# Performance work log

Hardware: AMD Instinct MI355X
Metric: run time of the kernel (lower is better)

Reference implementation:

```python
import jax, jax.numpy as jnp
import numpy as np


def _lstm_layer(x, w_ih, w_hh, b):
    """Single LSTM layer, PyTorch gate order (i, f, g, o).
    x: [B, T, Din]; w_ih: [4H, Din]; w_hh: [4H, H]; b: [4H] (= b_ih + b_hh).
    Returns hidden states [B, T, H]."""
    H = w_hh.shape[1]
    # Precompute input contribution for all timesteps at once (big GEMM).
    gates_x = jnp.einsum('btd,gd->btg', x, w_ih) + b  # [B, T, 4H]
    gates_t = jnp.swapaxes(gates_x, 0, 1)             # [T, B, 4H]
    B = x.shape[0]
    h0 = jnp.zeros((B, H), x.dtype)
    c0 = jnp.zeros((B, H), x.dtype)

    def step(carry, gx):
        h, c = carry
        g = gx + h @ w_hh.T                           # [B, 4H]
        i, f, gg, o = jnp.split(g, 4, axis=-1)
        i = jax.nn.sigmoid(i)
        f = jax.nn.sigmoid(f)
        gg = jnp.tanh(gg)
        o = jax.nn.sigmoid(o)
        c = f * c + i * gg
        h = o * jnp.tanh(c)
        return (h, c), h

    _, hs = jax.lax.scan(step, (h0, c0), gates_t)     # hs: [T, B, H]
    return jnp.swapaxes(hs, 0, 1)                     # [B, T, H]


def setup_inputs() -> dict:
    key = jax.random.key(0)
    ks = jax.random.split(key, 10)
    B, T, Din = 256, 256, 128
    Hemb = 512   # hidden_size (embed output)
    H = 512      # lstm_hidden_size
    L = 3        # nlayers
    Dout = 1     # output_size

    def unif(k, shape, bound):
        return jax.random.uniform(k, shape, jnp.float32, -bound, bound)

    s_emb = 1.0 / np.sqrt(Din)
    s_lstm = 1.0 / np.sqrt(H)
    s_dec = 1.0 / np.sqrt(H)

    return {
        'x': jax.random.normal(ks[0], (B, T, Din), jnp.float32),
        'embed_W': unif(ks[1], (Hemb, Din), s_emb),
        'embed_b': unif(ks[2], (Hemb,), s_emb),
        # stacked per-layer LSTM weights (hidden_size == lstm_hidden_size)
        'w_ih': unif(ks[3], (L, 4 * H, Hemb), s_lstm),
        'w_hh': unif(ks[4], (L, 4 * H, H), s_lstm),
        'b_ih': unif(ks[5], (L, 4 * H), s_lstm),
        'b_hh': unif(ks[6], (L, 4 * H), s_lstm),
        'dec_W': unif(ks[7], (Dout, H), s_dec),
        'dec_b': unif(ks[8], (Dout,), s_dec),
    }


def reference(x, embed_W, embed_b, w_ih, w_hh, b_ih, b_hh, dec_W, dec_b):
    # embed: Linear(input_size -> hidden_size)
    h = x @ embed_W.T + embed_b                       # [B, T, Hemb]
    # multi-layer LSTM (batch_first), zero initial state
    L = w_ih.shape[0]
    for l in range(L):
        h = _lstm_layer(h, w_ih[l], w_hh[l], b_ih[l] + b_hh[l])
    # decoder on last timestep, then flatten
    out = h[:, -1] @ dec_W.T + dec_b                  # [B, Dout]
    return out.reshape(-1)
```

## Files before the change

kernel.cpp:

```cpp
#include <hip/hip_runtime.h>
#include <hip/hip_fp16.h>
#include <cstdint>


#define TT   256
#define NBAT 256
#define DIN  128
#define HID  512

typedef _Float16 half_t;
typedef __attribute__((ext_vector_type(8))) _Float16 half8;
typedef __attribute__((ext_vector_type(4))) _Float16 half4v;
typedef __attribute__((ext_vector_type(4))) float f32x4;

__device__ __forceinline__ float sigmoidf_(float x) {
    return 1.f / (1.f + __expf(-x));
}
__device__ __forceinline__ float tanhf_(float x) {
    float xc = fminf(fmaxf(x, -15.f), 15.f);
    float e = __expf(2.f * xc);
    return (e - 1.f) / (e + 1.f);
}

__device__ __forceinline__ half8 ld_cg16(const half_t* p) {
    union { unsigned long long u[2]; half8 v; } r;
    r.u[0] = __hip_atomic_load((const unsigned long long*)p,
                               __ATOMIC_RELAXED, __HIP_MEMORY_SCOPE_AGENT);
    r.u[1] = __hip_atomic_load((const unsigned long long*)p + 1,
                               __ATOMIC_RELAXED, __HIP_MEMORY_SCOPE_AGENT);
    return r.v;
}
__device__ __forceinline__ void st_cg2(half_t* p, float v) {
    half_t h = (half_t)v;
    unsigned short b = __builtin_bit_cast(unsigned short, h);
    __hip_atomic_store((unsigned short*)p, b,
                       __ATOMIC_RELAXED, __HIP_MEMORY_SCOPE_AGENT);
}

__device__ __forceinline__ void phase_out2(float* Pl, const f32x4 acc[2][4],
                                           int wv, int lane) {
    #pragma unroll
    for (int m = 0; m < 2; ++m)
        #pragma unroll
        for (int n = 0; n < 4; ++n)
            #pragma unroll
            for (int q = 0; q < 4; ++q) {
                int prow = (wv << 5) + (m << 4) + ((lane >> 4) << 2) + q;
                int cidx = (n << 4) + (lane & 15);
                Pl[prow * 64 + (cidx ^ ((((prow >> 2) ^ prow) & 1) << 4))] = acc[m][n][q];
            }
}
__device__ __forceinline__ float red_gatesS(const float* Pl, const float* b4,
                                            int brow, int jj, float& c) {
    float gs[4];
    #pragma unroll
    for (int gt = 0; gt < 4; ++gt) {
        float s = b4[gt];
        int cidx = (gt << 4) + jj;
        #pragma unroll
        for (int w2 = 0; w2 < 4; ++w2) {
            int r0 = (w2 << 5) + brow;
            s += Pl[r0 * 64 + (cidx ^ ((((r0 >> 2) ^ r0) & 1) << 4))];
        }
        gs[gt] = s;
    }
    float ig = sigmoidf_(gs[0]), fg = sigmoidf_(gs[1]);
    float gg = tanhf_(gs[2]), og = sigmoidf_(gs[3]);
    c = fg * c + ig * gg;
    return og * tanhf_(c);
}

__global__ __launch_bounds__(256) void k_w16(const float* __restrict__ wih,
                                             const float* __restrict__ whh,
                                             half_t* __restrict__ wbuf) {
    half8* wb = (half8*)wbuf;
    const int bid = blockIdx.x;
    const int l = bid >> 7;
    const int rem = bid & 127;
    const int hb = rem >> 2, q = rem & 3;
    const int tid = threadIdx.x;
    #pragma unroll
    for (int i = 0; i < 8; ++i) {
        int unit = tid + (i << 8);
        int kit = unit >> 8, n = (unit >> 6) & 3, lane = unit & 63;
        int grow = l * 2048 + n * 512 + hb * 16 + (lane & 15);
        int col = q * 256 + kit * 32 + ((lane >> 4) << 3);
        const float* src = (col < 512) ? (wih + (size_t)grow * HID + col)
                                       : (whh + (size_t)grow * HID + (col - 512));
        float4 u0 = *(const float4*)src;
        float4 u1 = *(const float4*)(src + 4);
        wb[((size_t)(l * 32 + hb) * 4 + q) * 2048 + unit] =
            (half8){(half_t)u0.x, (half_t)u0.y, (half_t)u0.z, (half_t)u0.w,
                    (half_t)u1.x, (half_t)u1.y, (half_t)u1.z, (half_t)u1.w};
    }
}

__global__ __launch_bounds__(256) void k_embed(const float* __restrict__ x,
                                               const float* __restrict__ W,
                                               const float* __restrict__ bias,
                                               half_t* __restrict__ out) {
    extern __shared__ char smem[];
    half_t* Xs = (half_t*)smem;
    half_t* Ws = (half_t*)(smem + 16384);
    const int tid = threadIdx.x;
    const int bk = blockIdx.x;
    const int t = bk >> 2, b0 = (bk & 3) << 6;

    #pragma unroll
    for (int it = 0; it < 8; ++it) {
        int idx = tid + (it << 8);
        int r = idx >> 5, k = (idx & 31) << 2;
        float4 v = *(const float4*)(x + ((size_t)(b0 + r) * TT + t) * DIN + k);
        half4v hv = {(half_t)v.x, (half_t)v.y, (half_t)v.z, (half_t)v.w};
        int byte = r * 256 + ((k * 2) ^ ((r & 7) << 4));
        *(half4v*)((char*)Xs + byte) = hv;
    }
    #pragma unroll 4
    for (int it = 0; it < 64; ++it) {
        int idx = tid + (it << 8);
        int r = idx >> 5, k = (idx & 31) << 2;
        float4 v = *(const float4*)(W + (size_t)r * DIN + k);
        half4v hv = {(half_t)v.x, (half_t)v.y, (half_t)v.z, (half_t)v.w};
        int byte = r * 256 + ((k * 2) ^ ((r & 7) << 4));
        *(half4v*)((char*)Ws + byte) = hv;
    }
    __syncthreads();

    const int lane = tid & 63, wv = tid >> 6;
    f32x4 acc[4][8];
    #pragma unroll
    for (int m = 0; m < 4; ++m)
        #pragma unroll
        for (int n = 0; n < 8; ++n) acc[m][n] = (f32x4){0.f, 0.f, 0.f, 0.f};

    #pragma unroll
    for (int kit = 0; kit < 4; ++kit) {
        int kk = (kit << 5) + ((lane >> 4) << 3);
        half8 a[4];
        #pragma unroll
        for (int m = 0; m < 4; ++m) {
            int r = (m << 4) + (lane & 15);
            int byte = r * 256 + ((kk * 2) ^ ((r & 7) << 4));
            a[m] = *(half8*)((char*)Xs + byte);
        }
        #pragma unroll
        for (int n = 0; n < 8; ++n) {
            int r = (wv << 7) + (n << 4) + (lane & 15);
            int byte = r * 256 + ((kk * 2) ^ ((r & 7) << 4));
            half8 b = *(half8*)((char*)Ws + byte);
            #pragma unroll
            for (int m = 0; m < 4; ++m)
                acc[m][n] = __builtin_amdgcn_mfma_f32_16x16x32_f16(a[m], b, acc[m][n], 0, 0, 0);
        }
    }
    __syncthreads();
    half_t* Os = (half_t*)smem;
    #pragma unroll
    for (int n = 0; n < 8; ++n) {
        int j = (wv << 7) + (n << 4) + (lane & 15);
        float bj = bias[j];
        #pragma unroll
        for (int m = 0; m < 4; ++m)
            #pragma unroll
            for (int r = 0; r < 4; ++r) {
                int mr = (m << 4) + ((lane >> 4) << 2) + r;
                Os[mr * 512 + j] = (half_t)(acc[m][n][r] + bj);
            }
    }
    __syncthreads();
    #pragma unroll
    for (int it = 0; it < 16; ++it) {
        int idx = tid + (it << 8);
        int r = idx >> 6, c = (idx & 63) << 3;
        half8 v = *(half8*)(Os + r * 512 + c);
        *(half8*)(out + ((size_t)t * NBAT + (b0 + r)) * HID + c) = v;
    }
}

__global__ __launch_bounds__(256, 1) void k_rec(const half_t* __restrict__ wbuf,
                                                const half_t* __restrict__ bufE,
                                                half_t* __restrict__ ring0,
                                                half_t* __restrict__ ring1,
                                                half_t* __restrict__ ring2,
                                                half_t* __restrict__ outbuf,
                                                const float* __restrict__ b_ih,
                                                const float* __restrict__ b_hh,
                                                int* __restrict__ flags,
                                                int rdmask, int cached) {
    extern __shared__ char smem[];
    half8* W2s = (half8*)smem;
    float* Pl = (float*)(smem + 131072);

    const half8* wb = (const half8*)wbuf;
    const int tid = threadIdx.x;
    const int lane = tid & 63, wv = tid >> 6;
    const int g = blockIdx.x & 7;
    const int hb = blockIdx.x >> 3;
    const int b0 = g << 5;
    const int j0 = hb << 4;
    const int rr = tid >> 4;
    const int jj = tid & 15;
    const bool low = (wv < 2);
    const int qw = wv ^ 2;
    const int koff = ((wv & 1) << 8) + ((lane >> 4) << 3);
    bool dead = false;

    half8 Bf0[8][4], Bf1[8][4];
    {
        const half8* w0 = wb + ((size_t)hb * 4 + wv) * 2048;
        const half8* w1 = wb + ((size_t)(32 + hb) * 4 + qw) * 2048;
        #pragma unroll
        for (int kit = 0; kit < 8; ++kit)
            #pragma unroll
            for (int n = 0; n < 4; ++n) {
                Bf0[kit][n] = w0[kit * 256 + n * 64 + lane];
                Bf1[kit][n] = w1[kit * 256 + n * 64 + lane];
            }
    }
    {
        const half8* w2 = wb + (size_t)(64 + hb) * 4 * 2048;
        #pragma unroll 4
        for (int it = 0; it < 32; ++it) {
            int idx = tid + (it << 8);
            W2s[idx] = w2[idx];
        }
    }
    float bias[3][4];
    #pragma unroll
    for (int l = 0; l < 3; ++l)
        #pragma unroll
        for (int gt = 0; gt < 4; ++gt)
            bias[l][gt] = b_ih[(size_t)l * 2048 + gt * HID + j0 + jj] +
                          b_hh[(size_t)l * 2048 + gt * HID + j0 + jj];
    float cA0 = 0.f, cA1 = 0.f, cB0 = 0.f, cB1 = 0.f, cC0 = 0.f, cC1 = 0.f;
    __syncthreads();

    const size_t RNG = (size_t)NBAT * HID;

    for (int r = 0; r < TT + 2; ++r) {
        const bool act0 = (r < TT);
        const bool act1 = (r >= 1 && r <= TT);
        const bool act2 = (r >= 2);

        if (tid < 96 && !dead) {
            int l = tid >> 5;
            int need = r - l; if (need > TT) need = TT;
            if (need > 0) {
                const int* fp = flags + l * 256 + (g << 5) + (tid & 31);
                int guard = 0;
                while (__hip_atomic_load(fp, __ATOMIC_RELAXED,
                                         __HIP_MEMORY_SCOPE_AGENT) < need) {
                    __builtin_amdgcn_s_sleep(1);
                    if (++guard > (1 << 17)) { dead = true; break; }
                }
            }
        }
        __syncthreads();

        half8 p0a[8], p0b[8];
        const size_t rowb = (size_t)(b0 + (lane & 15)) * HID + koff;
        if (low) {
            if (act0) {
                const half_t* ar = bufE + (size_t)r * RNG + rowb;
                #pragma unroll
                for (int kit = 0; kit < 8; ++kit) {
                    p0a[kit] = *(const half8*)(ar + (kit << 5));
                    p0b[kit] = *(const half8*)(ar + (size_t)16 * HID + (kit << 5));
                }
            }
        } else if (act1) {
            const half_t* ar = ring0 + (size_t)((r - 1) & rdmask) * RNG + rowb;
            if (cached) {
                #pragma unroll
                for (int kit = 0; kit < 8; ++kit) {
                    p0a[kit] = *(const half8*)(ar + (kit << 5));
                    p0b[kit] = *(const half8*)(ar + (size_t)16 * HID + (kit << 5));
                }
            } else {
                #pragma unroll
                for (int kit = 0; kit < 8; ++kit) {
                    p0a[kit] = ld_cg16(ar + (kit << 5));
                    p0b[kit] = ld_cg16(ar + (size_t)16 * HID + (kit << 5));
                }
            }
        }

        f32x4 acc[2][4];

        #pragma unroll
        for (int m = 0; m < 2; ++m)
            #pragma unroll
            for (int n = 0; n < 4; ++n) acc[m][n] = (f32x4){0.f, 0.f, 0.f, 0.f};
        if (act0 && (low || r >= 1)) {
            #pragma unroll
            for (int kit = 0; kit < 8; ++kit)
                #pragma unroll
                for (int n = 0; n < 4; ++n) {
                    acc[0][n] = __builtin_amdgcn_mfma_f32_16x16x32_f16(p0a[kit], Bf0[kit][n], acc[0][n], 0, 0, 0);
                    acc[1][n] = __builtin_amdgcn_mfma_f32_16x16x32_f16(p0b[kit], Bf0[kit][n], acc[1][n], 0, 0, 0);
                }
        }
        half8 p1a[8], p1b[8];
        if (low && r >= 2) {
            const half_t* ar = ring1 + (size_t)((r - 2) & rdmask) * RNG + rowb;
            if (cached) {
                #pragma unroll
                for (int kit = 0; kit < 8; ++kit) {
                    p1a[kit] = *(const half8*)(ar + (kit << 5));
                    p1b[kit] = *(const half8*)(ar + (size_t)16 * HID + (kit << 5));
                }
            } else {
                #pragma unroll
                for (int kit = 0; kit < 8; ++kit) {
                    p1a[kit] = ld_cg16(ar + (kit << 5));
                    p1b[kit] = ld_cg16(ar + (size_t)16 * HID + (kit << 5));
                }
            }
        }
        {
            half_t* dst = ring0 + (size_t)(r & rdmask) * RNG;
            phase_out2(Pl, acc, wv, lane);
            __syncthreads();
            if (act0) {
                st_cg2(dst + (size_t)(b0 + rr) * HID + j0 + jj,
                       red_gatesS(Pl, bias[0], rr, jj, cA0));
                st_cg2(dst + (size_t)(b0 + 16 + rr) * HID + j0 + jj,
                       red_gatesS(Pl, bias[0], 16 + rr, jj, cA1));
            }
            __syncthreads();
        }

        #pragma unroll
        for (int m = 0; m < 2; ++m)
            #pragma unroll
            for (int n = 0; n < 4; ++n) acc[m][n] = (f32x4){0.f, 0.f, 0.f, 0.f};
        if (act1) {
            if (!low) {
                #pragma unroll
                for (int kit = 0; kit < 8; ++kit)
                    #pragma unroll
                    for (int n = 0; n < 4; ++n) {
                        acc[0][n] = __builtin_amdgcn_mfma_f32_16x16x32_f16(p0a[kit], Bf1[kit][n], acc[0][n], 0, 0, 0);
                        acc[1][n] = __builtin_amdgcn_mfma_f32_16x16x32_f16(p0b[kit], Bf1[kit][n], acc[1][n], 0, 0, 0);
                    }
            } else if (r >= 2) {
                #pragma unroll
                for (int kit = 0; kit < 8; ++kit)
                    #pragma unroll
                    for (int n = 0; n < 4; ++n) {
                        acc[0][n] = __builtin_amdgcn_mfma_f32_16x16x32_f16(p1a[kit], Bf1[kit][n], acc[0][n], 0, 0, 0);
                        acc[1][n] = __builtin_amdgcn_mfma_f32_16x16x32_f16(p1b[kit], Bf1[kit][n], acc[1][n], 0, 0, 0);
                    }
            }
        }
        if (!low && r >= 3) {
            const half_t* ar = ring2 + (size_t)((r - 3) & rdmask) * RNG + rowb;
            if (cached) {
                #pragma unroll
                for (int kit = 0; kit < 8; ++kit) {
                    p1a[kit] = *(const half8*)(ar + (kit << 5));
                    p1b[kit] = *(const half8*)(ar + (size_t)16 * HID + (kit << 5));
                }
            } else {
                #pragma unroll
                for (int kit = 0; kit < 8; ++kit) {
                    p1a[kit] = ld_cg16(ar + (kit << 5));
                    p1b[kit] = ld_cg16(ar + (size_t)16 * HID + (kit << 5));
                }
            }
        }
        {
            half_t* dst = ring1 + (size_t)((r - 1) & rdmask) * RNG;
            phase_out2(Pl, acc, wv, lane);
            __syncthreads();
            if (act1) {
                st_cg2(dst + (size_t)(b0 + rr) * HID + j0 + jj,
                       red_gatesS(Pl, bias[1], rr, jj, cB0));
                st_cg2(dst + (size_t)(b0 + 16 + rr) * HID + j0 + jj,
                       red_gatesS(Pl, bias[1], 16 + rr, jj, cB1));
            }
            __syncthreads();
        }

        #pragma unroll
        for (int m = 0; m < 2; ++m)
            #pragma unroll
            for (int n = 0; n < 4; ++n) acc[m][n] = (f32x4){0.f, 0.f, 0.f, 0.f};
        if (act2 && (low || r >= 3)) {
            const half8* w2l = W2s + ((size_t)wv << 11);
            #pragma unroll
            for (int kit = 0; kit < 8; ++kit) {
                half8 B0 = w2l[kit * 256 + 0 * 64 + lane];
                half8 B1 = w2l[kit * 256 + 1 * 64 + lane];
                half8 B2 = w2l[kit * 256 + 2 * 64 + lane];
                half8 B3 = w2l[kit * 256 + 3 * 64 + lane];
                acc[0][0] = __builtin_amdgcn_mfma_f32_16x16x32_f16(p1a[kit], B0, acc[0][0], 0, 0, 0);
                acc[1][0] = __builtin_amdgcn_mfma_f32_16x16x32_f16(p1b[kit], B0, acc[1][0], 0, 0, 0);
                acc[0][1] = __builtin_amdgcn_mfma_f32_16x16x32_f16(p1a[kit], B1, acc[0][1], 0, 0, 0);
                acc[1][1] = __builtin_amdgcn_mfma_f32_16x16x32_f16(p1b[kit], B1, acc[1][1], 0, 0, 0);
                acc[0][2] = __builtin_amdgcn_mfma_f32_16x16x32_f16(p1a[kit], B2, acc[0][2], 0, 0, 0);
                acc[1][2] = __builtin_amdgcn_mfma_f32_16x16x32_f16(p1b[kit], B2, acc[1][2], 0, 0, 0);
                acc[0][3] = __builtin_amdgcn_mfma_f32_16x16x32_f16(p1a[kit], B3, acc[0][3], 0, 0, 0);
                acc[1][3] = __builtin_amdgcn_mfma_f32_16x16x32_f16(p1b[kit], B3, acc[1][3], 0, 0, 0);
            }
        }
        {
            const int t2 = r - 2;
            half_t* dst = ring2 + (size_t)(t2 & rdmask) * RNG;
            phase_out2(Pl, acc, wv, lane);
            __syncthreads();
            if (act2) {
                float h0v = red_gatesS(Pl, bias[2], rr, jj, cC0);
                float h1v = red_gatesS(Pl, bias[2], 16 + rr, jj, cC1);
                st_cg2(dst + (size_t)(b0 + rr) * HID + j0 + jj, h0v);
                st_cg2(dst + (size_t)(b0 + 16 + rr) * HID + j0 + jj, h1v);
                if (t2 == TT - 1) {
                    st_cg2(outbuf + (size_t)(b0 + rr) * HID + j0 + jj, h0v);
                    st_cg2(outbuf + (size_t)(b0 + 16 + rr) * HID + j0 + jj, h1v);
                }
            }
        }

        asm volatile("s_waitcnt vmcnt(0)" ::: "memory");
        __builtin_amdgcn_sched_barrier(0);
        __syncthreads();
        if (tid == 0 && act0)
            __hip_atomic_store(flags + 0 * 256 + (g << 5) + hb, r + 1,
                               __ATOMIC_RELAXED, __HIP_MEMORY_SCOPE_AGENT);
        if (tid == 1 && act1)
            __hip_atomic_store(flags + 1 * 256 + (g << 5) + hb, r,
                               __ATOMIC_RELAXED, __HIP_MEMORY_SCOPE_AGENT);
        if (tid == 2 && act2)
            __hip_atomic_store(flags + 2 * 256 + (g << 5) + hb, r - 1,
                               __ATOMIC_RELAXED, __HIP_MEMORY_SCOPE_AGENT);
    }
}

__global__ __launch_bounds__(256) void k_dec(const half_t* __restrict__ act,
                                             const float* __restrict__ dW,
                                             const float* __restrict__ db,
                                             float* __restrict__ out) {
    int tid = threadIdx.x;
    int bl = tid >> 3, part = tid & 7;
    int b = (blockIdx.x << 5) + bl;
    const half_t* row = act + (size_t)b * HID + (part << 6);
    float s = 0.f;
    #pragma unroll
    for (int i = 0; i < 8; ++i) {
        half8 v = ld_cg16(row + (i << 3));
        const float* wp = dW + (part << 6) + (i << 3);
        #pragma unroll
        for (int u = 0; u < 8; ++u) s += (float)v[u] * wp[u];
    }
    #pragma unroll
    for (int off = 1; off < 8; off <<= 1) s += __shfl_xor(s, off, 64);
    if (part == 0) out[b] = s + db[0];
}

extern "C" void kernel_launch(void* const* d_in, const int* in_sizes, int n_in,
                              void* d_out, int out_size, void* d_ws, size_t ws_size,
                              hipStream_t stream) {
    const float* x = (const float*)d_in[0];
    const float* eW = (const float*)d_in[1];
    const float* eb = (const float*)d_in[2];
    const float* wih = (const float*)d_in[3];
    const float* whh = (const float*)d_in[4];
    const float* bih = (const float*)d_in[5];
    const float* bhh = (const float*)d_in[6];
    const float* dW = (const float*)d_in[7];
    const float* db = (const float*)d_in[8];
    float* out = (float*)d_out;

    const size_t MB = 1u << 20;
    const size_t RINGFULL = 64 * MB;
    const size_t FULL_NEED = 270 * MB + 65536;
    const bool full = (ws_size >= FULL_NEED);
    if (ws_size < 96 * MB + 65536) return;

    char* ws = (char*)d_ws;
    half_t* bufE = (half_t*)ws;
    half_t *ring0, *ring1, *ring2, *outbuf, *wbuf;
    int* flags;
    int rdmask, cached;
    if (full) {
        ring0 = (half_t*)(ws + 64 * MB);
        ring1 = (half_t*)(ws + 128 * MB);
        ring2 = (half_t*)(ws + 192 * MB);
        outbuf = (half_t*)(ws + 256 * MB);
        wbuf = (half_t*)(ws + 257 * MB);
        flags = (int*)(ws + 270 * MB);
        rdmask = 255; cached = 1;
    } else {
        ring0 = (half_t*)(ws + 64 * MB);
        ring1 = (half_t*)(ws + 68 * MB);
        ring2 = (half_t*)(ws + 72 * MB);
        outbuf = (half_t*)(ws + 76 * MB);
        wbuf = (half_t*)(ws + 80 * MB);
        flags = (int*)(ws + 96 * MB);
        rdmask = 15; cached = 0;
    }

    hipMemsetAsync(flags, 0, 1024 * sizeof(int), stream);

    (void)hipFuncSetAttribute((const void*)k_embed,
                              hipFuncAttributeMaxDynamicSharedMemorySize, 147456);
    (void)hipFuncSetAttribute((const void*)k_rec,
                              hipFuncAttributeMaxDynamicSharedMemorySize, 163840);

    k_w16<<<384, 256, 0, stream>>>(wih, whh, wbuf);
    k_embed<<<1024, 256, 147456, stream>>>(x, eW, eb, bufE);

    void* args[] = { (void*)&wbuf, (void*)&bufE, (void*)&ring0, (void*)&ring1,
                     (void*)&ring2, (void*)&outbuf, (void*)&bih, (void*)&bhh,
                     (void*)&flags, (void*)&rdmask, (void*)&cached };
    hipError_t ce = hipLaunchCooperativeKernel((const void*)k_rec, dim3(256), dim3(256),
                                               args, 163840, stream);
    if (ce != hipSuccess) {
        k_rec<<<256, 256, 163840, stream>>>(wbuf, bufE, ring0, ring1, ring2,
                                            outbuf, bih, bhh, flags, rdmask, cached);
    }

    k_dec<<<8, 256, 0, stream>>>(outbuf, dW, db, out);
}
```

Before: 2.944 ms.

## Replace per-block flag polling with per-group atomic counters and a fixed 16-slot ring

Inter-block synchronization moves from 32 per-producer flags polled by 96 threads to one atomic counter per batch group and layer, incremented with fetch_add and polled by 3 threads. Consumers wait until the counter reaches 32 times the required step. The large-workspace path (256-deep ring with plain cached loads) is dropped, so the kernel always uses a 16-deep ring with cache-bypassing loads. This cuts polling traffic and per-step wait latency, but atomic contention on the shared counters rises and the cached-load path is lost when the workspace is large.

Measured after the change: 3.569 ms. 1.21x slower.

```diff
diff --git a/kernel.cpp b/kernel.cpp
--- a/kernel.cpp
+++ b/kernel.cpp
@@ -7,6 +7,7 @@
 #define NBAT 256
 #define DIN  128
 #define HID  512
+#define RD   16
 
 typedef _Float16 half_t;
 typedef __attribute__((ext_vector_type(8))) _Float16 half8;
@@ -185,8 +186,7 @@
                                                 half_t* __restrict__ outbuf,
                                                 const float* __restrict__ b_ih,
                                                 const float* __restrict__ b_hh,
-                                                int* __restrict__ flags,
-                                                int rdmask, int cached) {
+                                                int* __restrict__ counts) {
     extern __shared__ char smem[];
     half8* W2s = (half8*)smem;
     float* Pl = (float*)(smem + 131072);
@@ -242,14 +242,15 @@
         const bool act1 = (r >= 1 && r <= TT);
         const bool act2 = (r >= 2);
 
-        if (tid < 96 && !dead) {
-            int l = tid >> 5;
+        if (tid < 3 && !dead) {
+            int l = tid;
             int need = r - l; if (need > TT) need = TT;
             if (need > 0) {
-                const int* fp = flags + l * 256 + (g << 5) + (tid & 31);
+                const int* cp = counts + l * 8 + g;
+                const int want = need << 5;
                 int guard = 0;
-                while (__hip_atomic_load(fp, __ATOMIC_RELAXED,
-                                         __HIP_MEMORY_SCOPE_AGENT) < need) {
+                while (__hip_atomic_load(cp, __ATOMIC_RELAXED,
+                                         __HIP_MEMORY_SCOPE_AGENT) < want) {
                     __builtin_amdgcn_s_sleep(1);
                     if (++guard > (1 << 17)) { dead = true; break; }
                 }
@@ -269,19 +270,11 @@
                 }
             }
         } else if (act1) {
-            const half_t* ar = ring0 + (size_t)((r - 1) & rdmask) * RNG + rowb;
-            if (cached) {
-                #pragma unroll
-                for (int kit = 0; kit < 8; ++kit) {
-                    p0a[kit] = *(const half8*)(ar + (kit << 5));
-                    p0b[kit] = *(const half8*)(ar + (size_t)16 * HID + (kit << 5));
-                }
-            } else {
-                #pragma unroll
-                for (int kit = 0; kit < 8; ++kit) {
-                    p0a[kit] = ld_cg16(ar + (kit << 5));
-                    p0b[kit] = ld_cg16(ar + (size_t)16 * HID + (kit << 5));
-                }
+            const half_t* ar = ring0 + (size_t)((r - 1) & (RD - 1)) * RNG + rowb;
+            #pragma unroll
+            for (int kit = 0; kit < 8; ++kit) {
+                p0a[kit] = ld_cg16(ar + (kit << 5));
+                p0b[kit] = ld_cg16(ar + (size_t)16 * HID + (kit << 5));
             }
         }
 
@@ -302,23 +295,15 @@
         }
         half8 p1a[8], p1b[8];
         if (low && r >= 2) {
-            const half_t* ar = ring1 + (size_t)((r - 2) & rdmask) * RNG + rowb;
-            if (cached) {
-                #pragma unroll
-                for (int kit = 0; kit < 8; ++kit) {
-                    p1a[kit] = *(const half8*)(ar + (kit << 5));
-                    p1b[kit] = *(const half8*)(ar + (size_t)16 * HID + (kit << 5));
-                }
-            } else {
-                #pragma unroll
-                for (int kit = 0; kit < 8; ++kit) {
-                    p1a[kit] = ld_cg16(ar + (kit << 5));
-                    p1b[kit] = ld_cg16(ar + (size_t)16 * HID + (kit << 5));
-                }
+            const half_t* ar = ring1 + (size_t)((r - 2) & (RD - 1)) * RNG + rowb;
+            #pragma unroll
+            for (int kit = 0; kit < 8; ++kit) {
+                p1a[kit] = ld_cg16(ar + (kit << 5));
+                p1b[kit] = ld_cg16(ar + (size_t)16 * HID + (kit << 5));
             }
         }
         {
-            half_t* dst = ring0 + (size_t)(r & rdmask) * RNG;
+            half_t* dst = ring0 + (size_t)(r & (RD - 1)) * RNG;
             phase_out2(Pl, acc, wv, lane);
             __syncthreads();
             if (act0) {
@@ -354,23 +339,15 @@
             }
         }
         if (!low && r >= 3) {
-            const half_t* ar = ring2 + (size_t)((r - 3) & rdmask) * RNG + rowb;
-            if (cached) {
-                #pragma unroll
-                for (int kit = 0; kit < 8; ++kit) {
-                    p1a[kit] = *(const half8*)(ar + (kit << 5));
-                    p1b[kit] = *(const half8*)(ar + (size_t)16 * HID + (kit << 5));
-                }
-            } else {
-                #pragma unroll
-                for (int kit = 0; kit < 8; ++kit) {
-                    p1a[kit] = ld_cg16(ar + (kit << 5));
-                    p1b[kit] = ld_cg16(ar + (size_t)16 * HID + (kit << 5));
-                }
+            const half_t* ar = ring2 + (size_t)((r - 3) & (RD - 1)) * RNG + rowb;
+            #pragma unroll
+            for (int kit = 0; kit < 8; ++kit) {
+                p1a[kit] = ld_cg16(ar + (kit << 5));
+                p1b[kit] = ld_cg16(ar + (size_t)16 * HID + (kit << 5));
             }
         }
         {
-            half_t* dst = ring1 + (size_t)((r - 1) & rdmask) * RNG;
+            half_t* dst = ring1 + (size_t)((r - 1) & (RD - 1)) * RNG;
             phase_out2(Pl, acc, wv, lane);
             __syncthreads();
             if (act1) {
@@ -406,7 +383,7 @@
         }
         {
             const int t2 = r - 2;
-            half_t* dst = ring2 + (size_t)(t2 & rdmask) * RNG;
+            half_t* dst = ring2 + (size_t)(t2 & (RD - 1)) * RNG;
             phase_out2(Pl, acc, wv, lane);
             __syncthreads();
             if (act2) {
@@ -425,14 +402,14 @@
         __builtin_amdgcn_sched_barrier(0);
         __syncthreads();
         if (tid == 0 && act0)
-            __hip_atomic_store(flags + 0 * 256 + (g << 5) + hb, r + 1,
-                               __ATOMIC_RELAXED, __HIP_MEMORY_SCOPE_AGENT);
+            __hip_atomic_fetch_add(counts + 0 * 8 + g, 1,
+                                   __ATOMIC_RELAXED, __HIP_MEMORY_SCOPE_AGENT);
         if (tid == 1 && act1)
-            __hip_atomic_store(flags + 1 * 256 + (g << 5) + hb, r,
-                               __ATOMIC_RELAXED, __HIP_MEMORY_SCOPE_AGENT);
+            __hip_atomic_fetch_add(counts + 1 * 8 + g, 1,
+                                   __ATOMIC_RELAXED, __HIP_MEMORY_SCOPE_AGENT);
         if (tid == 2 && act2)
-            __hip_atomic_store(flags + 2 * 256 + (g << 5) + hb, r - 1,
-                               __ATOMIC_RELAXED, __HIP_MEMORY_SCOPE_AGENT);
+            __hip_atomic_fetch_add(counts + 2 * 8 + g, 1,
+                                   __ATOMIC_RELAXED, __HIP_MEMORY_SCOPE_AGENT);
     }
 }
 
@@ -472,35 +449,18 @@
     float* out = (float*)d_out;
 
     const size_t MB = 1u << 20;
-    const size_t RINGFULL = 64 * MB;
-    const size_t FULL_NEED = 270 * MB + 65536;
-    const bool full = (ws_size >= FULL_NEED);
     if (ws_size < 96 * MB + 65536) return;
 
     char* ws = (char*)d_ws;
     half_t* bufE = (half_t*)ws;
-    half_t *ring0, *ring1, *ring2, *outbuf, *wbuf;
-    int* flags;
-    int rdmask, cached;
-    if (full) {
-        ring0 = (half_t*)(ws + 64 * MB);
-        ring1 = (half_t*)(ws + 128 * MB);
-        ring2 = (half_t*)(ws + 192 * MB);
-        outbuf = (half_t*)(ws + 256 * MB);
-        wbuf = (half_t*)(ws + 257 * MB);
-        flags = (int*)(ws + 270 * MB);
-        rdmask = 255; cached = 1;
-    } else {
-        ring0 = (half_t*)(ws + 64 * MB);
-        ring1 = (half_t*)(ws + 68 * MB);
-        ring2 = (half_t*)(ws + 72 * MB);
-        outbuf = (half_t*)(ws + 76 * MB);
-        wbuf = (half_t*)(ws + 80 * MB);
-        flags = (int*)(ws + 96 * MB);
-        rdmask = 15; cached = 0;
-    }
-
-    hipMemsetAsync(flags, 0, 1024 * sizeof(int), stream);
+    half_t* ring0 = (half_t*)(ws + 64 * MB);
+    half_t* ring1 = (half_t*)(ws + 68 * MB);
+    half_t* ring2 = (half_t*)(ws + 72 * MB);
+    half_t* outbuf = (half_t*)(ws + 76 * MB);
+    half_t* wbuf = (half_t*)(ws + 80 * MB);
+    int* counts = (int*)(ws + 96 * MB);
+
+    hipMemsetAsync(counts, 0, 1024 * sizeof(int), stream);
 
     (void)hipFuncSetAttribute((const void*)k_embed,
                               hipFuncAttributeMaxDynamicSharedMemorySize, 147456);
@@ -512,12 +472,12 @@
 
     void* args[] = { (void*)&wbuf, (void*)&bufE, (void*)&ring0, (void*)&ring1,
                      (void*)&ring2, (void*)&outbuf, (void*)&bih, (void*)&bhh,
-                     (void*)&flags, (void*)&rdmask, (void*)&cached };
+                     (void*)&counts };
     hipError_t ce = hipLaunchCooperativeKernel((const void*)k_rec, dim3(256), dim3(256),
                                                args, 163840, stream);
     if (ce != hipSuccess) {
         k_rec<<<256, 256, 163840, stream>>>(wbuf, bufE, ring0, ring1, ring2,
-                                            outbuf, bih, bhh, flags, rdmask, cached);
+                                            outbuf, bih, bhh, counts);
     }
 
     k_dec<<<8, 256, 0, stream>>>(outbuf, dW, db, out);
```
